# Optimization experiments

Measured on AMD Instinct MI355X. Metric: run time of the kernel, lower is better.

Reference implementation:

```python
import jax, jax.numpy as jnp
import numpy as np

D_MODEL = 1024
NUM_HEADS = 16
HEAD_DIM = D_MODEL // NUM_HEADS
ROPE_THETA = 10000.0


def apply_rope(x, pos):
    # x: [B, H, S, Dh]; pos: [S] int. Interleaved-pair rotary embedding.
    d = x.shape[-1]
    inv_freq = 1.0 / (ROPE_THETA ** (jnp.arange(0, d, 2, dtype=jnp.float32) / d))  # [Dh/2]
    ang = pos.astype(jnp.float32)[:, None] * inv_freq[None, :]  # [S, Dh/2]
    cos, sin = jnp.cos(ang), jnp.sin(ang)
    x1 = x[..., 0::2]
    x2 = x[..., 1::2]
    r1 = x1 * cos - x2 * sin
    r2 = x1 * sin + x2 * cos
    return jnp.stack([r1, r2], axis=-1).reshape(x.shape)


def setup_inputs() -> dict:
    key = jax.random.key(0)
    ks = jax.random.split(key, 5)
    B, S = 4, 2048
    x = jax.random.normal(ks[0], (B, S, D_MODEL), dtype=jnp.float32)
    token_positions = jnp.arange(S, dtype=jnp.int32)
    scale = 1.0 / np.sqrt(D_MODEL)
    wq = jax.random.normal(ks[1], (D_MODEL, D_MODEL), dtype=jnp.float32) * scale
    wk = jax.random.normal(ks[2], (D_MODEL, D_MODEL), dtype=jnp.float32) * scale
    wv = jax.random.normal(ks[3], (D_MODEL, D_MODEL), dtype=jnp.float32) * scale
    wo = jax.random.normal(ks[4], (D_MODEL, D_MODEL), dtype=jnp.float32) * scale
    return {"x": x, "token_positions": token_positions, "wq": wq, "wk": wk, "wv": wv, "wo": wo}


def reference(x, token_positions, wq, wk, wv, wo):
    B, S, D = x.shape
    # Linear: einsum('d_out d_in, ... d_in -> ... d_out')
    def proj(w, t):
        return jnp.einsum('oi,bsi->bso', w, t)
    q = proj(wq, x).reshape(B, S, NUM_HEADS, HEAD_DIM).transpose(0, 2, 1, 3)  # [B,H,S,Dh]
    k = proj(wk, x).reshape(B, S, NUM_HEADS, HEAD_DIM).transpose(0, 2, 1, 3)
    v = proj(wv, x).reshape(B, S, NUM_HEADS, HEAD_DIM).transpose(0, 2, 1, 3)
    q = apply_rope(q, token_positions)
    k = apply_rope(k, token_positions)
    scores = jnp.einsum('bhqd,bhkd->bhqk', q, k) / jnp.sqrt(jnp.float32(HEAD_DIM))
    causal = jnp.tril(jnp.ones((S, S), dtype=bool))  # True = keep
    scores = jnp.where(causal, scores, -jnp.inf)
    attn = jax.nn.softmax(scores, axis=-1)
    out = jnp.einsum('bhqk,bhkd->bhqd', attn, v)  # [B,H,S,Dh]
    out = out.transpose(0, 2, 1, 3).reshape(B, S, D)
    return jnp.einsum('oi,bsi->bso', wo, out)
```

## Files before the change

kernel.cpp:

```cpp
#include <hip/hip_runtime.h>
#include <hip/hip_fp16.h>

#define DM   1024
#define NH   16
#define HD   64
#define BATCH 4
#define SEQ  2048
#define MROWS (BATCH*SEQ)
#define BHSD  ((size_t)BATCH*NH*SEQ*HD)

using f32x4 = __attribute__((ext_vector_type(4))) float;
using f16x8 = __attribute__((ext_vector_type(8))) _Float16;
using f16x4 = __attribute__((ext_vector_type(4))) _Float16;
using fp16x2 = __attribute__((ext_vector_type(2))) __fp16;
using u32x2 = __attribute__((ext_vector_type(2))) unsigned int;

__device__ __forceinline__ void gload_lds16(const void* g, void* l) {
    __builtin_amdgcn_global_load_lds(
        (const __attribute__((address_space(1))) void*)g,
        (__attribute__((address_space(3))) void*)l, 16, 0, 0);
}

__device__ __forceinline__ float red16_max(float v) {
    u32x2 r = __builtin_amdgcn_permlane16_swap(__float_as_uint(v), __float_as_uint(v), false, false);
    return fmaxf(__uint_as_float(r[0]), __uint_as_float(r[1]));
}
__device__ __forceinline__ float red32_max(float v) {
    u32x2 r = __builtin_amdgcn_permlane32_swap(__float_as_uint(v), __float_as_uint(v), false, false);
    return fmaxf(__uint_as_float(r[0]), __uint_as_float(r[1]));
}
__device__ __forceinline__ float red16_add(float v) {
    u32x2 r = __builtin_amdgcn_permlane16_swap(__float_as_uint(v), __float_as_uint(v), false, false);
    return __uint_as_float(r[0]) + __uint_as_float(r[1]);
}
__device__ __forceinline__ float red32_add(float v) {
    u32x2 r = __builtin_amdgcn_permlane32_swap(__float_as_uint(v), __float_as_uint(v), false, false);
    return __uint_as_float(r[0]) + __uint_as_float(r[1]);
}

__global__ __launch_bounds__(256) void f32_to_f16(const float* __restrict__ in,
                                                  _Float16* __restrict__ out, int n) {
    int i = (blockIdx.x * 256 + threadIdx.x) * 4;
    if (i >= n) return;
    float4 v = *(const float4*)(in + i);
    union { _Float16 h[4]; ushort4 u; } cv;
    cv.h[0] = (_Float16)v.x; cv.h[1] = (_Float16)v.y;
    cv.h[2] = (_Float16)v.z; cv.h[3] = (_Float16)v.w;
    *(ushort4*)(out + i) = cv.u;
}

__global__ __launch_bounds__(256) void rope_table(const int* __restrict__ pos,
                                                  float2* __restrict__ tab) {
    int idx = blockIdx.x * 256 + threadIdx.x;
    int s = idx >> 5, j = idx & 31;
    float p = (float)pos[s];
    float invf = powf(10000.0f, -(float)j / 32.0f);
    float ang = p * invf;
    tab[idx] = make_float2(cosf(ang), sinf(ang));
}

template<int MODE>
__global__ __launch_bounds__(256)
void gemm_f16(const _Float16* __restrict__ A, const _Float16* __restrict__ Bw,
              float* __restrict__ outF, _Float16* __restrict__ qkv,
              const float2* __restrict__ rope) {
    __shared__ __align__(16) _Float16 lds[2][2][128][32];
    const int tid  = threadIdx.x;
    const int lane = tid & 63;
    const int wid  = tid >> 6;
    const int m0 = blockIdx.x * 128;
    const int n0 = blockIdx.y * 128;
    const int wm = (wid >> 1) * 64;
    const int wn = (wid & 1) * 64;
    const int g   = lane >> 4;
    const int r16 = lane & 15;

    const int srow0 = (wid*2 + 0)*16 + (lane >> 2);
    const int srow1 = (wid*2 + 1)*16 + (lane >> 2);
    const int sch0 = (lane & 3) ^ ((srow0 >> 1) & 3);
    const int sch1 = (lane & 3) ^ ((srow1 >> 1) & 3);
    const _Float16* Asrc0 = A  + (size_t)(m0 + srow0)*DM + sch0*8;
    const _Float16* Asrc1 = A  + (size_t)(m0 + srow1)*DM + sch1*8;
    const _Float16* Bsrc0 = Bw + (size_t)(n0 + srow0)*DM + sch0*8;
    const _Float16* Bsrc1 = Bw + (size_t)(n0 + srow1)*DM + sch1*8;

    f32x4 acc[4][4] = {};

    #define STAGE(buf, kt) do {                                           \
        const int koff = (kt)*32;                                         \
        _Float16* bA = &lds[(buf)][0][0][0];                              \
        _Float16* bB = &lds[(buf)][1][0][0];                              \
        gload_lds16(Asrc0 + koff, bA + (wid*2 + 0)*512);                  \
        gload_lds16(Asrc1 + koff, bA + (wid*2 + 1)*512);                  \
        gload_lds16(Bsrc0 + koff, bB + (wid*2 + 0)*512);                  \
        gload_lds16(Bsrc1 + koff, bB + (wid*2 + 1)*512);                  \
    } while (0)

    STAGE(0, 0);
    for (int kt = 0; kt < 32; ++kt) {
        __syncthreads();
        if (kt + 1 < 32) STAGE((kt + 1) & 1, kt + 1);
        const int buf = kt & 1;
        f16x8 af[4], bf[4];
        #pragma unroll
        for (int i = 0; i < 4; ++i) {
            int rowa = wm + i*16 + r16;
            af[i] = *(const f16x8*)&lds[buf][0][rowa][(g ^ ((rowa >> 1) & 3)) * 8];
            int rowb = wn + i*16 + r16;
            bf[i] = *(const f16x8*)&lds[buf][1][rowb][(g ^ ((rowb >> 1) & 3)) * 8];
        }
        #pragma unroll
        for (int i = 0; i < 4; ++i)
            #pragma unroll
            for (int j = 0; j < 4; ++j)
                acc[i][j] = __builtin_amdgcn_mfma_f32_16x16x32_f16(af[i], bf[j], acc[i][j], 0, 0, 0);
    }
    #undef STAGE

    #pragma unroll
    for (int i = 0; i < 4; ++i) {
        #pragma unroll
        for (int j = 0; j < 4; ++j) {
            if constexpr (MODE == 0) {
                #pragma unroll
                for (int r = 0; r < 4; ++r) {
                    const int m = m0 + wm + i*16 + g*4 + r;
                    const int n = n0 + wn + j*16 + r16;
                    outF[(size_t)m*DM + n] = acc[i][j][r];
                }
            } else {
                const int n = n0 + wn + j*16 + r16;
                const int sel = n >> 10;
                const int cc = n & 1023;
                const int h = cc >> 6, dd = cc & 63;
                if (sel == 2) {
                    const int mb = m0 + wm + i*16 + g*4;
                    const int s0 = mb & (SEQ - 1), b = mb >> 11;
                    f16x4 pk;
                    #pragma unroll
                    for (int r = 0; r < 4; ++r) pk[r] = (_Float16)acc[i][j][r];
                    *(f16x4*)(qkv + 2*BHSD + ((size_t)((b*NH + h)*HD + dd))*SEQ + s0) = pk;
                } else {
                    #pragma unroll
                    for (int r = 0; r < 4; ++r) {
                        const int m = m0 + wm + i*16 + g*4 + r;
                        float v = acc[i][j][r];
                        float vp = __shfl_xor(v, 1);
                        const int s = m & (SEQ - 1), b = m >> 11;
                        float2 cs = rope[(s << 5) + (dd >> 1)];
                        float o;
                        if (dd & 1) o = vp * cs.y + v * cs.x;
                        else        o = v * cs.x - vp * cs.y;
                        if (sel == 0) o *= 0.18033688f;
                        qkv[(size_t)sel*BHSD + ((size_t)((b*NH + h)*SEQ + s))*HD + dd] = (_Float16)o;
                    }
                }
            }
        }
    }
}

__device__ __forceinline__ void process_tile(
    const _Float16 (*__restrict__ Klb)[64], const _Float16 (*__restrict__ Vlb)[64],
    const f16x8 (&qf)[2], f32x4 (&ot)[4], float &m, float &l,
    const int Rq, const int kv0, const int g, const int r16) {

    f32x4 sT[4] = {};
    const int kchunkBase = r16 & 7;
    __builtin_amdgcn_s_setprio(1);
    #pragma unroll
    for (int ks = 0; ks < 2; ++ks) {
        #pragma unroll
        for (int n = 0; n < 4; ++n) {
            f16x8 kf = *(const f16x8*)&Klb[n*16 + r16][(((ks<<2)|g) ^ kchunkBase)*8];
            sT[n] = __builtin_amdgcn_mfma_f32_16x16x32_f16(kf, qf[ks], sT[n], 0, 0, 0);
        }
    }
    __builtin_amdgcn_s_setprio(0);

    const bool full = (kv0 + 63 <= Rq);
    float sv[16];
    if (full) {
        #pragma unroll
        for (int n = 0; n < 4; ++n)
            #pragma unroll
            for (int r = 0; r < 4; ++r) sv[n*4 + r] = sT[n][r];
    } else {
        const int q = Rq + r16;
        #pragma unroll
        for (int n = 0; n < 4; ++n)
            #pragma unroll
            for (int r = 0; r < 4; ++r)
                sv[n*4 + r] = (kv0 + n*16 + 4*g + r <= q) ? sT[n][r] : -INFINITY;
    }
    float mx = sv[0];
    #pragma unroll
    for (int i = 1; i < 16; ++i) mx = fmaxf(mx, sv[i]);
    mx = red32_max(red16_max(mx));
    const bool need = (mx > m + 8.f);
    if (__any(need)) {
        float mnew = need ? mx : m;
        float al = exp2f(m - mnew);
        m = mnew;
        l *= al;
        #pragma unroll
        for (int n = 0; n < 4; ++n) ot[n] *= al;
    }
    float ps = 0.f;
    #pragma unroll
    for (int i = 0; i < 16; ++i) { sv[i] = exp2f(sv[i] - m); ps += sv[i]; }
    l += red32_add(red16_add(ps));

    uint pk[4][2];
    #pragma unroll
    for (int t = 0; t < 4; ++t)
        #pragma unroll
        for (int rp = 0; rp < 2; ++rp) {
            union { fp16x2 h; uint u; } cv;
            cv.h = __builtin_amdgcn_cvt_pkrtz(sv[t*4 + 2*rp], sv[t*4 + 2*rp + 1]);
            pk[t][rp] = cv.u;
        }
    uint w[2][4];
    #pragma unroll
    for (int kk = 0; kk < 2; ++kk)
        #pragma unroll
        for (int rp = 0; rp < 2; ++rp) {
            u32x2 s32 = __builtin_amdgcn_permlane32_swap(pk[2*kk][rp], pk[2*kk + 1][rp], false, false);
            u32x2 s16 = __builtin_amdgcn_permlane16_swap(s32[0], s32[1], false, false);
            w[kk][rp]     = s16[0];
            w[kk][2 + rp] = s16[1];
        }

    __builtin_amdgcn_s_setprio(1);
    #pragma unroll
    for (int ks = 0; ks < 2; ++ks) {
        union { uint u[4]; f16x8 h; } pb;
        #pragma unroll
        for (int j2 = 0; j2 < 4; ++j2) pb.u[j2] = w[ks][j2];
        #pragma unroll
        for (int n = 0; n < 4; ++n) {
            f16x8 vf = *(const f16x8*)&Vlb[n*16 + r16][(((ks<<2)|g) ^ kchunkBase)*8];
            ot[n] = __builtin_amdgcn_mfma_f32_16x16x32_f16(vf, pb.h, ot[n], 0, 0, 0);
        }
    }
    __builtin_amdgcn_s_setprio(0);
}

__global__ __launch_bounds__(256, 4)
void attn_kernel(const _Float16* __restrict__ qkv, _Float16* __restrict__ ao) {
    const int tid = threadIdx.x, lane = tid & 63, w = tid >> 6;
    const int g = lane >> 4, r16 = lane & 15;
    const int bh = blockIdx.x;
    const int jq = blockIdx.y;
    const int q0h = (31 - jq) * 64, q0l = jq * 64;
    const _Float16* Q   = qkv + (size_t)bh * SEQ * HD;
    const _Float16* Kp  = qkv + BHSD + (size_t)bh * SEQ * HD;
    const _Float16* Vpt = qkv + 2*BHSD + (size_t)bh * SEQ * HD;

    __shared__ __align__(16) _Float16 Kl[2][64][64];
    __shared__ __align__(16) _Float16 Vl[2][64][64];

    const int rA = tid >> 3,        rB = 32 + (tid >> 3);
    const int lcA = (tid & 7) ^ (rA & 7), lcB = (tid & 7) ^ (rB & 7);
    const _Float16* KsrcA = Kp  + (size_t)rA*HD + lcA*8;
    const _Float16* KsrcB = Kp  + (size_t)rB*HD + lcB*8;
    const _Float16* VsrcA = Vpt + (size_t)rA*SEQ + lcA*8;
    const _Float16* VsrcB = Vpt + (size_t)rB*SEQ + lcB*8;

    const int Rh = q0h + w*16, Rl = q0l + w*16;
    f16x8 qfh[2], qfl[2];
    #pragma unroll
    for (int ks = 0; ks < 2; ++ks) {
        qfh[ks] = *(const f16x8*)(Q + (size_t)(Rh + r16)*HD + ks*32 + g*8);
        qfl[ks] = *(const f16x8*)(Q + (size_t)(Rl + r16)*HD + ks*32 + g*8);
    }

    f32x4 oth[4] = {}, otl[4] = {};
    float mh = -INFINITY, lh = 0.f, ml_ = -INFINITY, ll_ = 0.f;

    const int nth = (q0h >> 6) + 1;
    const int ntl = (q0l >> 6) + 1;

    #define STAGE(buf, kv0) do {                                              \
        gload_lds16(KsrcA + (size_t)(kv0)*HD, &Kl[(buf)][0][0] + tid*8);      \
        gload_lds16(KsrcB + (size_t)(kv0)*HD, &Kl[(buf)][0][0] + (256+tid)*8);\
        gload_lds16(VsrcA + (kv0),            &Vl[(buf)][0][0] + tid*8);      \
        gload_lds16(VsrcB + (kv0),            &Vl[(buf)][0][0] + (256+tid)*8);\
    } while (0)

    STAGE(0, 0);
    for (int kt = 0; kt < nth; ++kt) {
        const int kv0 = kt << 6;
        __syncthreads();
        if (kt + 1 < nth) STAGE((kt + 1) & 1, (kt + 1) << 6);
        const int buf = kt & 1;

        if (kv0 <= Rh + 15)
            process_tile(Kl[buf], Vl[buf], qfh, oth, mh, lh, Rh, kv0, g, r16);
        if (kt < ntl)
            process_tile(Kl[buf], Vl[buf], qfl, otl, ml_, ll_, Rl, kv0, g, r16);
    }
    #undef STAGE

    const int b = bh >> 4, h = bh & 15;
    const float invh = 1.0f / lh, invl = 1.0f / ll_;
    _Float16* dsth = ao + ((size_t)(b*SEQ + Rh + r16))*DM + h*HD + g*4;
    _Float16* dstl = ao + ((size_t)(b*SEQ + Rl + r16))*DM + h*HD + g*4;
    #pragma unroll
    for (int n = 0; n < 4; ++n) {
        f16x4 pkh, pkl;
        #pragma unroll
        for (int r = 0; r < 4; ++r) {
            pkh[r] = (_Float16)(oth[n][r] * invh);
            pkl[r] = (_Float16)(otl[n][r] * invl);
        }
        *(f16x4*)(dsth + n*16) = pkh;
        *(f16x4*)(dstl + n*16) = pkl;
    }
}

extern "C" void kernel_launch(void* const* d_in, const int* in_sizes, int n_in,
                              void* d_out, int out_size, void* d_ws, size_t ws_size,
                              hipStream_t stream) {
    const float* x  = (const float*)d_in[0];
    const int*   tp = (const int*)d_in[1];
    const float* wq = (const float*)d_in[2];
    const float* wk = (const float*)d_in[3];
    const float* wv = (const float*)d_in[4];
    const float* wo = (const float*)d_in[5];
    float* out = (float*)d_out;

    char* ws = (char*)d_ws;
    _Float16* xh  = (_Float16*)(ws);
    _Float16* whq = (_Float16*)(ws + 16777216);
    _Float16* woh = (_Float16*)(ws + 23068672);
    _Float16* qkv = (_Float16*)(ws + 25165824);
    _Float16* ao  = (_Float16*)(ws + 75497472);
    float2*   rope= (float2*)  (ws + 92274688);

    f32_to_f16<<<MROWS*DM/1024, 256, 0, stream>>>(x, xh, MROWS*DM);
    f32_to_f16<<<DM*DM/1024, 256, 0, stream>>>(wq, whq,            DM*DM);
    f32_to_f16<<<DM*DM/1024, 256, 0, stream>>>(wk, whq + DM*DM,    DM*DM);
    f32_to_f16<<<DM*DM/1024, 256, 0, stream>>>(wv, whq + 2*DM*DM,  DM*DM);
    f32_to_f16<<<DM*DM/1024, 256, 0, stream>>>(wo, woh,            DM*DM);
    rope_table<<<SEQ*32/256, 256, 0, stream>>>(tp, rope);

    gemm_f16<1><<<dim3(MROWS/128, 3*DM/128), 256, 0, stream>>>(xh, whq, nullptr, qkv, rope);
    attn_kernel<<<dim3(BATCH*NH, 16), 256, 0, stream>>>(qkv, ao);
    gemm_f16<0><<<dim3(MROWS/128, DM/128), 256, 0, stream>>>(ao, woh, out, nullptr, nullptr);
}
```

Before: 216.0 us.

## Rewrite projection GEMMs as 8-wave 256x128 tiles with ping-pong scheduling

Replaces the 4-wave 128x128 GEMM with a 512-thread kernel that computes 256x128 tiles using a K-step of 64 and an XOR-swizzled LDS layout. The main loop splits each K tile into two halves, with explicit barriers, s_setprio around MFMA bursts, and manual vmcnt waits so global-to-LDS prefetch of tile t+2 overlaps compute. It targets better MFMA utilisation and more data reuse per block. The cost is more LDS per block, fewer blocks for the output projection, and fragile hand-tuned wait counts.

Result: faster. 207.3 us (-4.0%).

```diff
diff --git a/kernel.cpp b/kernel.cpp
--- a/kernel.cpp
+++ b/kernel.cpp
@@ -60,60 +60,106 @@
 }
 
 template<int MODE>
-__global__ __launch_bounds__(256)
-void gemm_f16(const _Float16* __restrict__ A, const _Float16* __restrict__ Bw,
-              float* __restrict__ outF, _Float16* __restrict__ qkv,
-              const float2* __restrict__ rope) {
-    __shared__ __align__(16) _Float16 lds[2][2][128][32];
+__global__ __launch_bounds__(512, 2)
+void gemm8p(const _Float16* __restrict__ A, const _Float16* __restrict__ Bw,
+            float* __restrict__ outF, _Float16* __restrict__ qkv,
+            const float2* __restrict__ rope) {
+    constexpr int NK = DM / 64;
+    __shared__ __align__(16) _Float16 ldsA[2][256][64];
+    __shared__ __align__(16) _Float16 ldsB[2][128][64];
     const int tid  = threadIdx.x;
     const int lane = tid & 63;
     const int wid  = tid >> 6;
-    const int m0 = blockIdx.x * 128;
+    const int m0 = blockIdx.x * 256;
     const int n0 = blockIdx.y * 128;
     const int wm = (wid >> 1) * 64;
     const int wn = (wid & 1) * 64;
     const int g   = lane >> 4;
     const int r16 = lane & 15;
-
-    const int srow0 = (wid*2 + 0)*16 + (lane >> 2);
-    const int srow1 = (wid*2 + 1)*16 + (lane >> 2);
-    const int sch0 = (lane & 3) ^ ((srow0 >> 1) & 3);
-    const int sch1 = (lane & 3) ^ ((srow1 >> 1) & 3);
-    const _Float16* Asrc0 = A  + (size_t)(m0 + srow0)*DM + sch0*8;
-    const _Float16* Asrc1 = A  + (size_t)(m0 + srow1)*DM + sch1*8;
-    const _Float16* Bsrc0 = Bw + (size_t)(n0 + srow0)*DM + sch0*8;
-    const _Float16* Bsrc1 = Bw + (size_t)(n0 + srow1)*DM + sch1*8;
+    const int cx  = r16 & 7;
+
+    const _Float16* srcA[4];
+    int dstA[4];
+    #pragma unroll
+    for (int L = 0; L < 4; ++L) {
+        const int u = L*512 + tid, row = u >> 3, c = (u & 7) ^ (row & 7);
+        srcA[L] = A + (size_t)(m0 + row)*DM + c*8;
+        dstA[L] = u*8;
+    }
+    const _Float16* srcB[2];
+    int dstB[2];
+    #pragma unroll
+    for (int L = 0; L < 2; ++L) {
+        const int u = L*512 + tid, row = u >> 3, c = (u & 7) ^ (row & 7);
+        srcB[L] = Bw + (size_t)(n0 + row)*DM + c*8;
+        dstB[L] = u*8;
+    }
+    _Float16* lAf = &ldsA[0][0][0];
+    _Float16* lBf = &ldsB[0][0][0];
+
+    #define STAGE(cur, kt) do {                                        \
+        const int ko = (kt)*64;                                        \
+        gload_lds16(srcA[0] + ko, lAf + (cur)*16384 + dstA[0]);        \
+        gload_lds16(srcA[1] + ko, lAf + (cur)*16384 + dstA[1]);        \
+        gload_lds16(srcA[2] + ko, lAf + (cur)*16384 + dstA[2]);        \
+        gload_lds16(srcA[3] + ko, lAf + (cur)*16384 + dstA[3]);        \
+        gload_lds16(srcB[0] + ko, lBf + (cur)*8192 + dstB[0]);         \
+        gload_lds16(srcB[1] + ko, lBf + (cur)*8192 + dstB[1]);         \
+    } while (0)
 
     f32x4 acc[4][4] = {};
 
-    #define STAGE(buf, kt) do {                                           \
-        const int koff = (kt)*32;                                         \
-        _Float16* bA = &lds[(buf)][0][0][0];                              \
-        _Float16* bB = &lds[(buf)][1][0][0];                              \
-        gload_lds16(Asrc0 + koff, bA + (wid*2 + 0)*512);                  \
-        gload_lds16(Asrc1 + koff, bA + (wid*2 + 1)*512);                  \
-        gload_lds16(Bsrc0 + koff, bB + (wid*2 + 0)*512);                  \
-        gload_lds16(Bsrc1 + koff, bB + (wid*2 + 1)*512);                  \
-    } while (0)
-
     STAGE(0, 0);
-    for (int kt = 0; kt < 32; ++kt) {
-        __syncthreads();
-        if (kt + 1 < 32) STAGE((kt + 1) & 1, kt + 1);
-        const int buf = kt & 1;
-        f16x8 af[4], bf[4];
-        #pragma unroll
-        for (int i = 0; i < 4; ++i) {
-            int rowa = wm + i*16 + r16;
-            af[i] = *(const f16x8*)&lds[buf][0][rowa][(g ^ ((rowa >> 1) & 3)) * 8];
-            int rowb = wn + i*16 + r16;
-            bf[i] = *(const f16x8*)&lds[buf][1][rowb][(g ^ ((rowb >> 1) & 3)) * 8];
-        }
+    STAGE(1, 1);
+    asm volatile("s_waitcnt vmcnt(6)" ::: "memory");
+    __builtin_amdgcn_s_barrier();
+
+    for (int t = 0; t < NK; ++t) {
+        const int cur = t & 1;
+        const _Float16* lA = lAf + cur*16384;
+        const _Float16* lB = lBf + cur*8192;
+
+        f16x8 a0[4], b0[4];
+        #pragma unroll
+        for (int i = 0; i < 4; ++i)
+            a0[i] = *(const f16x8*)(lA + (wm + i*16 + r16)*64 + ((g ^ cx) * 8));
+        #pragma unroll
+        for (int j = 0; j < 4; ++j)
+            b0[j] = *(const f16x8*)(lB + (wn + j*16 + r16)*64 + ((g ^ cx) * 8));
+        asm volatile("s_waitcnt lgkmcnt(0)" ::: "memory");
+        __builtin_amdgcn_sched_barrier(0);
+        __builtin_amdgcn_s_barrier();
+        __builtin_amdgcn_s_setprio(1);
         #pragma unroll
         for (int i = 0; i < 4; ++i)
             #pragma unroll
             for (int j = 0; j < 4; ++j)
-                acc[i][j] = __builtin_amdgcn_mfma_f32_16x16x32_f16(af[i], bf[j], acc[i][j], 0, 0, 0);
+                acc[i][j] = __builtin_amdgcn_mfma_f32_16x16x32_f16(a0[i], b0[j], acc[i][j], 0, 0, 0);
+        __builtin_amdgcn_s_setprio(0);
+        __builtin_amdgcn_s_barrier();
+
+        f16x8 a1[4], b1[4];
+        #pragma unroll
+        for (int i = 0; i < 4; ++i)
+            a1[i] = *(const f16x8*)(lA + (wm + i*16 + r16)*64 + (((4|g) ^ cx) * 8));
+        #pragma unroll
+        for (int j = 0; j < 4; ++j)
+            b1[j] = *(const f16x8*)(lB + (wn + j*16 + r16)*64 + (((4|g) ^ cx) * 8));
+        asm volatile("s_waitcnt lgkmcnt(0)" ::: "memory");
+        __builtin_amdgcn_sched_barrier(0);
+        __builtin_amdgcn_s_barrier();
+        if (t + 2 < NK) STAGE(cur, t + 2);
+        __builtin_amdgcn_s_setprio(1);
+        #pragma unroll
+        for (int i = 0; i < 4; ++i)
+            #pragma unroll
+            for (int j = 0; j < 4; ++j)
+                acc[i][j] = __builtin_amdgcn_mfma_f32_16x16x32_f16(a1[i], b1[j], acc[i][j], 0, 0, 0);
+        __builtin_amdgcn_s_setprio(0);
+        if (t + 2 < NK)      asm volatile("s_waitcnt vmcnt(6)" ::: "memory");
+        else if (t == NK-2)  asm volatile("s_waitcnt vmcnt(0)" ::: "memory");
+        __builtin_amdgcn_sched_barrier(0);
+        __builtin_amdgcn_s_barrier();
     }
     #undef STAGE
 
@@ -345,7 +391,7 @@
     f32_to_f16<<<DM*DM/1024, 256, 0, stream>>>(wo, woh,            DM*DM);
     rope_table<<<SEQ*32/256, 256, 0, stream>>>(tp, rope);
 
-    gemm_f16<1><<<dim3(MROWS/128, 3*DM/128), 256, 0, stream>>>(xh, whq, nullptr, qkv, rope);
+    gemm8p<1><<<dim3(MROWS/256, 3*DM/128), 512, 0, stream>>>(xh, whq, nullptr, qkv, rope);
     attn_kernel<<<dim3(BATCH*NH, 16), 256, 0, stream>>>(qkv, ao);
-    gemm_f16<0><<<dim3(MROWS/128, DM/128), 256, 0, stream>>>(ao, woh, out, nullptr, nullptr);
-}
+    gemm8p<0><<<dim3(MROWS/256, DM/128), 512, 0, stream>>>(ao, woh, out, nullptr, nullptr);
+}
```

## Share K/V fragment loads across both query tiles and merge cast kernels

Applied to the files above, without the earlier changes.

The attention inner loop now processes the high and low query tiles together: K and V fragments are read from LDS once and fed to the MFMAs for both tiles, and the two softmax steps are interleaved. This cuts LDS read traffic and gives the scheduler more independent work, at the cost of more live registers under the occupancy-4 launch bound. The five separate fp32-to-fp16 cast launches become one kernel that dispatches by index, and the GEMM MFMA loop gets raised wave priority.

Result: faster. 202.5 us (-6.2%).

```diff
diff --git a/kernel.cpp b/kernel.cpp
--- a/kernel.cpp
+++ b/kernel.cpp
@@ -38,15 +38,26 @@
     return __uint_as_float(r[0]) + __uint_as_float(r[1]);
 }
 
-__global__ __launch_bounds__(256) void f32_to_f16(const float* __restrict__ in,
-                                                  _Float16* __restrict__ out, int n) {
-    int i = (blockIdx.x * 256 + threadIdx.x) * 4;
-    if (i >= n) return;
-    float4 v = *(const float4*)(in + i);
+__global__ __launch_bounds__(256) void cast_all(
+    const float* __restrict__ x,  const float* __restrict__ wq,
+    const float* __restrict__ wk, const float* __restrict__ wv,
+    const float* __restrict__ wo, _Float16* __restrict__ xh,
+    _Float16* __restrict__ whq,   _Float16* __restrict__ woh) {
+    const int i = (blockIdx.x * 256 + threadIdx.x) * 4;
+    const float* src; _Float16* dst; int off;
+    if (i < MROWS*DM) { src = x; dst = xh; off = i; }
+    else {
+        int j = i - MROWS*DM;
+        int sel = j >> 20;
+        off = j & (DM*DM - 1);
+        src = (sel == 0) ? wq : (sel == 1) ? wk : (sel == 2) ? wv : wo;
+        dst = (sel == 3) ? woh : (whq + (size_t)sel * DM * DM);
+    }
+    float4 v = *(const float4*)(src + off);
     union { _Float16 h[4]; ushort4 u; } cv;
     cv.h[0] = (_Float16)v.x; cv.h[1] = (_Float16)v.y;
     cv.h[2] = (_Float16)v.z; cv.h[3] = (_Float16)v.w;
-    *(ushort4*)(out + i) = cv.u;
+    *(ushort4*)(dst + off) = cv.u;
 }
 
 __global__ __launch_bounds__(256) void rope_table(const int* __restrict__ pos,
@@ -109,11 +120,13 @@
             int rowb = wn + i*16 + r16;
             bf[i] = *(const f16x8*)&lds[buf][1][rowb][(g ^ ((rowb >> 1) & 3)) * 8];
         }
+        __builtin_amdgcn_s_setprio(1);
         #pragma unroll
         for (int i = 0; i < 4; ++i)
             #pragma unroll
             for (int j = 0; j < 4; ++j)
                 acc[i][j] = __builtin_amdgcn_mfma_f32_16x16x32_f16(af[i], bf[j], acc[i][j], 0, 0, 0);
+        __builtin_amdgcn_s_setprio(0);
     }
     #undef STAGE
 
@@ -160,23 +173,9 @@
     }
 }
 
-__device__ __forceinline__ void process_tile(
-    const _Float16 (*__restrict__ Klb)[64], const _Float16 (*__restrict__ Vlb)[64],
-    const f16x8 (&qf)[2], f32x4 (&ot)[4], float &m, float &l,
-    const int Rq, const int kv0, const int g, const int r16) {
-
-    f32x4 sT[4] = {};
-    const int kchunkBase = r16 & 7;
-    __builtin_amdgcn_s_setprio(1);
-    #pragma unroll
-    for (int ks = 0; ks < 2; ++ks) {
-        #pragma unroll
-        for (int n = 0; n < 4; ++n) {
-            f16x8 kf = *(const f16x8*)&Klb[n*16 + r16][(((ks<<2)|g) ^ kchunkBase)*8];
-            sT[n] = __builtin_amdgcn_mfma_f32_16x16x32_f16(kf, qf[ks], sT[n], 0, 0, 0);
-        }
-    }
-    __builtin_amdgcn_s_setprio(0);
+__device__ __forceinline__ void softmax_frag(
+    const f32x4 (&sT)[4], f32x4 (&ot)[4], float &m, float &l,
+    const int Rq, const int kv0, const int g, const int r16, uint (&w)[2][4]) {
 
     const bool full = (kv0 + 63 <= Rq);
     float sv[16];
@@ -220,7 +219,6 @@
             cv.h = __builtin_amdgcn_cvt_pkrtz(sv[t*4 + 2*rp], sv[t*4 + 2*rp + 1]);
             pk[t][rp] = cv.u;
         }
-    uint w[2][4];
     #pragma unroll
     for (int kk = 0; kk < 2; ++kk)
         #pragma unroll
@@ -230,17 +228,61 @@
             w[kk][rp]     = s16[0];
             w[kk][2 + rp] = s16[1];
         }
-
+}
+
+__device__ __forceinline__ void process_tile2(
+    const _Float16 (*__restrict__ Klb)[64], const _Float16 (*__restrict__ Vlb)[64],
+    const f16x8 (&qfh)[2], const f16x8 (&qfl)[2],
+    f32x4 (&oth)[4], f32x4 (&otl)[4],
+    float &mh, float &lh, float &ml, float &ll,
+    const int Rh, const int Rl, const bool doLo,
+    const int kv0, const int g, const int r16) {
+
+    const int kchunkBase = r16 & 7;
+
+    f32x4 sTh[4] = {}, sTl[4] = {};
     __builtin_amdgcn_s_setprio(1);
     #pragma unroll
     for (int ks = 0; ks < 2; ++ks) {
-        union { uint u[4]; f16x8 h; } pb;
-        #pragma unroll
-        for (int j2 = 0; j2 < 4; ++j2) pb.u[j2] = w[ks][j2];
-        #pragma unroll
-        for (int n = 0; n < 4; ++n) {
-            f16x8 vf = *(const f16x8*)&Vlb[n*16 + r16][(((ks<<2)|g) ^ kchunkBase)*8];
-            ot[n] = __builtin_amdgcn_mfma_f32_16x16x32_f16(vf, pb.h, ot[n], 0, 0, 0);
+        f16x8 kf[4];
+        #pragma unroll
+        for (int n = 0; n < 4; ++n)
+            kf[n] = *(const f16x8*)&Klb[n*16 + r16][(((ks<<2)|g) ^ kchunkBase)*8];
+        #pragma unroll
+        for (int n = 0; n < 4; ++n)
+            sTh[n] = __builtin_amdgcn_mfma_f32_16x16x32_f16(kf[n], qfh[ks], sTh[n], 0, 0, 0);
+        if (doLo) {
+            #pragma unroll
+            for (int n = 0; n < 4; ++n)
+                sTl[n] = __builtin_amdgcn_mfma_f32_16x16x32_f16(kf[n], qfl[ks], sTl[n], 0, 0, 0);
+        }
+    }
+    __builtin_amdgcn_s_setprio(0);
+
+    uint wh[2][4], wl[2][4];
+    softmax_frag(sTh, oth, mh, lh, Rh, kv0, g, r16, wh);
+    if (doLo) softmax_frag(sTl, otl, ml, ll, Rl, kv0, g, r16, wl);
+
+    __builtin_amdgcn_s_setprio(1);
+    #pragma unroll
+    for (int ks = 0; ks < 2; ++ks) {
+        f16x8 vf[4];
+        #pragma unroll
+        for (int n = 0; n < 4; ++n)
+            vf[n] = *(const f16x8*)&Vlb[n*16 + r16][(((ks<<2)|g) ^ kchunkBase)*8];
+        union { uint u[4]; f16x8 h; } pbh;
+        #pragma unroll
+        for (int j2 = 0; j2 < 4; ++j2) pbh.u[j2] = wh[ks][j2];
+        #pragma unroll
+        for (int n = 0; n < 4; ++n)
+            oth[n] = __builtin_amdgcn_mfma_f32_16x16x32_f16(vf[n], pbh.h, oth[n], 0, 0, 0);
+        if (doLo) {
+            union { uint u[4]; f16x8 h; } pbl;
+            #pragma unroll
+            for (int j2 = 0; j2 < 4; ++j2) pbl.u[j2] = wl[ks][j2];
+            #pragma unroll
+            for (int n = 0; n < 4; ++n)
+                otl[n] = __builtin_amdgcn_mfma_f32_16x16x32_f16(vf[n], pbl.h, otl[n], 0, 0, 0);
         }
     }
     __builtin_amdgcn_s_setprio(0);
@@ -295,10 +337,8 @@
         if (kt + 1 < nth) STAGE((kt + 1) & 1, (kt + 1) << 6);
         const int buf = kt & 1;
 
-        if (kv0 <= Rh + 15)
-            process_tile(Kl[buf], Vl[buf], qfh, oth, mh, lh, Rh, kv0, g, r16);
-        if (kt < ntl)
-            process_tile(Kl[buf], Vl[buf], qfl, otl, ml_, ll_, Rl, kv0, g, r16);
+        process_tile2(Kl[buf], Vl[buf], qfh, qfl, oth, otl,
+                      mh, lh, ml_, ll_, Rh, Rl, (kt < ntl), kv0, g, r16);
     }
     #undef STAGE
 
@@ -338,11 +378,7 @@
     _Float16* ao  = (_Float16*)(ws + 75497472);
     float2*   rope= (float2*)  (ws + 92274688);
 
-    f32_to_f16<<<MROWS*DM/1024, 256, 0, stream>>>(x, xh, MROWS*DM);
-    f32_to_f16<<<DM*DM/1024, 256, 0, stream>>>(wq, whq,            DM*DM);
-    f32_to_f16<<<DM*DM/1024, 256, 0, stream>>>(wk, whq + DM*DM,    DM*DM);
-    f32_to_f16<<<DM*DM/1024, 256, 0, stream>>>(wv, whq + 2*DM*DM,  DM*DM);
-    f32_to_f16<<<DM*DM/1024, 256, 0, stream>>>(wo, woh,            DM*DM);
+    cast_all<<<(MROWS*DM + 4*DM*DM)/1024, 256, 0, stream>>>(x, wq, wk, wv, wo, xh, whq, woh);
     rope_table<<<SEQ*32/256, 256, 0, stream>>>(tp, rope);
 
     gemm_f16<1><<<dim3(MROWS/128, 3*DM/128), 256, 0, stream>>>(xh, whq, nullptr, qkv, rope);
```
